# Kernel tuning notes

Measured on AMD Instinct MI355X. Metric: run time of the kernel, lower is better.

## Reference

```python
import jax, jax.numpy as jnp
import numpy as np

T, B, L, H, IN = 256, 64, 4, 1024, 1024


def setup_inputs() -> dict:
    key = jax.random.key(0)
    k1, k2, k3 = jax.random.split(key, 3)
    x = jax.random.normal(k1, (T, B, IN), dtype=jnp.float32)
    h = jnp.zeros((L, B, H), dtype=jnp.float32)
    # nn.Linear default init: U(-1/sqrt(fan_in), 1/sqrt(fan_in)), fan_in = IN + H
    bound = 1.0 / np.sqrt(IN + H)
    # Stacked per-layer weights: W[l] is [IN+H, 2H] (transposed vs torch), b[l] is [2H]
    W = jax.random.uniform(k2, (L, IN + H, 2 * H), dtype=jnp.float32, minval=-bound, maxval=bound)
    b = jax.random.uniform(k3, (L, 2 * H), dtype=jnp.float32, minval=-bound, maxval=bound)
    return {"x": x, "h": h, "W": W, "b": b}


def reference(x, h, W, b):
    """SRU-cell stacked RNN.
    x: [T, B, IN]; h: [L, B, H]; W: [L, IN+H, 2H]; b: [L, 2H].
    Returns (outputs [T, B, H], h_final [L*B, H]) matching the torch module
    (torch.cat(h, 0) concatenates layer states along the batch axis).
    """
    num_layers = W.shape[0]

    def step(hs, x_t):  # hs: [L, B, H], x_t: [B, IN]
        inp = x_t
        new_hs = []
        for i in range(num_layers):
            z = jnp.concatenate([inp, hs[i]], axis=-1) @ W[i] + b[i]  # [B, 2H]
            learn, forget = jnp.split(z, 2, axis=-1)
            f = jax.nn.sigmoid(forget)
            hn = f * hs[i] + (1.0 - f) * jnp.tanh(learn)  # [B, H]
            new_hs.append(hn)
            inp = hn  # cell output is both next-layer input and new hidden
        return jnp.stack(new_hs), inp

    h_final, outputs = jax.lax.scan(step, h, x)
    return outputs, h_final.reshape(-1, h_final.shape[-1])
```

## Files before the change

### kernel.cpp

```cpp
#include <hip/hip_runtime.h>


typedef _Float16 f16;
typedef _Float16 f16x8 __attribute__((ext_vector_type(8)));
typedef _Float16 f16x4 __attribute__((ext_vector_type(4)));
typedef float    floatx4 __attribute__((ext_vector_type(4)));

#define T_ 256
#define B_ 64
#define L_ 4
#define H_ 1024
#define IN_ 1024
#define K_ 2048

#define PANEL (B_*H_)
#define RING_BYTES ((size_t)L_*T_*PANEL*2)
#define CTRL_OFF   RING_BYTES
#define CTRL_BYTES 4096
#define X16_OFF    (CTRL_OFF + 65536)

__global__ void convert_x_kernel(const float* __restrict__ x, f16* __restrict__ x16) {
  const int nvec = (T_*B_*IN_)/4;
  const int stride = gridDim.x*blockDim.x;
  for (int v = blockIdx.x*blockDim.x + threadIdx.x; v < nvec; v += stride) {
    floatx4 in = ((const floatx4*)x)[v];
    f16x4 o; o.x = (f16)in.x; o.y = (f16)in.y; o.z = (f16)in.z; o.w = (f16)in.w;
    ((f16x4*)x16)[v] = o;
  }
}

template<int CSLP, int FSLP, bool SLACK>
__device__ __forceinline__ unsigned poll_bk(const unsigned int* line, unsigned tgt) {
  const unsigned int* p = line + (threadIdx.x & 63);
  unsigned v = __hip_atomic_load(p, __ATOMIC_RELAXED, __HIP_MEMORY_SCOPE_SYSTEM);
  if (!__all((int)(v >= tgt))) {
    __builtin_amdgcn_s_sleep(CSLP);
    for (;;) {
      v = __hip_atomic_load(p, __ATOMIC_RELAXED, __HIP_MEMORY_SCOPE_SYSTEM);
      if (__all((int)(v >= tgt))) break;
      __builtin_amdgcn_s_sleep(FSLP);
    }
  }
  unsigned a = tgt;
  if (SLACK) {
    if      (__all((int)(v >= tgt + 16))) a = tgt + 16;
    else if (__all((int)(v >= tgt + 4)))  a = tgt + 4;
    else if (__all((int)(v >= tgt + 1)))  a = tgt + 1;
  }
  asm volatile("" ::: "memory");
  return a;
}

__global__ __launch_bounds__(512, 2) void sru_main(
    const float* __restrict__ W,
    const float* __restrict__ bias,
    const f16*  __restrict__ x16,
    f16*        __restrict__ ring,
    unsigned int* __restrict__ done,
    float*      __restrict__ out)
{
  __shared__ f16 Wt[32][2048];
  __shared__ float red[2][4][2][64][4];
  __shared__ f16 hst[64][24];

  const int bid  = blockIdx.x;
  const int l    = bid >> 6;
  const int c    = bid & 63;
  const int n0   = c*16;
  const int tid  = threadIdx.x;
  const int lane = tid & 63;
  const int quad = lane >> 4;
  const int lc   = lane & 15;
  const int w    = tid >> 6;
  const int kh   = w & 1;
  const int mh   = (w >> 1) & 1;
  const int rh   = w >> 2;
  const int R    = rh*32 + mh*16;
  const int grp  = rh*2 + mh;

  {
    const int jj = tid & 15;
    const int k0 = tid >> 4;
    const int x0 = (jj & 7) << 3;
    const float* Wl = W + (size_t)l*K_*2048;
    for (int i = 0; i < 64; ++i) {
      int k = k0 + i*32;
      int ks = k ^ x0;
      Wt[jj][ks]      = (f16)Wl[(size_t)k*2048 + n0 + jj];
      Wt[16 + jj][ks] = (f16)Wl[(size_t)k*2048 + 1024 + n0 + jj];
    }
  }
  const float bl = bias[l*2048 + n0 + lc];
  const float bf = bias[l*2048 + 1024 + n0 + lc];
  __syncthreads();

  floatx4 hreg = 0.f;

  unsigned int* lineL = done + ((l*4 + grp) << 6);
  unsigned int* lineP = (l > 0) ? done + (((l-1)*4 + grp) << 6) : (unsigned int*)0;
  unsigned avail = 0;

  const int xr  = (lc & 7) << 3;
  const int sw0 = (quad*8) ^ xr;
  const int sw1 = (32 + quad*8) ^ xr;
  const int kb  = kh*1024;
  const f16* bL0 = &Wt[lc][sw0];
  const f16* bL1 = &Wt[lc][sw1];
  const f16* bF0 = &Wt[16 + lc][sw0];
  const f16* bF1 = &Wt[16 + lc][sw1];

  for (int t = 0; t < T_; ++t) {
    if (kh == 0) {
      if (l > 0 && avail < (unsigned)(t+1))
        avail = poll_bk<16, 4, true>(lineP, (unsigned)(t+1));
    } else {
      if (t > 0) (void)poll_bk<32, 4, false>(lineL, (unsigned)t);
    }

    floatx4 accLa = 0.f, accLb = 0.f, accFa = 0.f, accFb = 0.f;

    if (!(kh == 1 && t == 0)) {
      const f16* Abase;
      if (kh == 1)      Abase = ring + (size_t)(l*T_ + (t-1))*PANEL;
      else if (l == 0)  Abase = x16 + (size_t)t*PANEL;
      else              Abase = ring + (size_t)((l-1)*T_ + t)*PANEL;
      const f16* ap = Abase + (size_t)(R + lc)*H_ + quad*8;

      #pragma unroll
      for (int g = 0; g < 4; ++g) {
        floatx4 ar[8];
        #pragma unroll
        for (int j = 0; j < 8; ++j)
          ar[j] = *(const floatx4*)(ap + (g*8 + j)*32);
        #pragma unroll
        for (int j = 0; j < 8; ++j) {
          const int m = (g*8 + j) >> 1;
          const f16* pL = (j & 1) ? bL1 : bL0;
          const f16* pF = (j & 1) ? bF1 : bF0;
          f16x8 av = __builtin_bit_cast(f16x8, ar[j]);
          f16x8 bL = *(const f16x8*)(pL + kb + m*64);
          f16x8 bF = *(const f16x8*)(pF + kb + m*64);
          if (g & 1) {
            accLb = __builtin_amdgcn_mfma_f32_16x16x32_f16(av, bL, accLb, 0,0,0);
            accFb = __builtin_amdgcn_mfma_f32_16x16x32_f16(av, bF, accFb, 0,0,0);
          } else {
            accLa = __builtin_amdgcn_mfma_f32_16x16x32_f16(av, bL, accLa, 0,0,0);
            accFa = __builtin_amdgcn_mfma_f32_16x16x32_f16(av, bF, accFa, 0,0,0);
          }
        }
      }
    }

    if (kh == 1) {
      *(floatx4*)&red[t&1][grp][0][lane][0] = accLa + accLb;
      *(floatx4*)&red[t&1][grp][1][lane][0] = accFa + accFb;
    }
    __syncthreads();

    if (kh == 0) {
      floatx4 zL = accLa + accLb + *(const floatx4*)&red[t&1][grp][0][lane][0];
      floatx4 zF = accFa + accFb + *(const floatx4*)&red[t&1][grp][1][lane][0];
      f16* ringw = ring + (size_t)(l*T_ + t)*PANEL;

      #pragma unroll
      for (int r = 0; r < 4; ++r) {
        float zl = zL[r] + bl;
        float zf = zF[r] + bf;
        float fg = 1.0f/(1.0f + __expf(-zf));
        float th = 1.0f - 2.0f/(__expf(2.0f*zl) + 1.0f);
        float hn = fg*hreg[r] + (1.0f - fg)*th;
        hreg[r] = hn;
        hst[R + quad*4 + r][lc] = (f16)hn;
      }
      asm volatile("s_waitcnt lgkmcnt(0)" ::: "memory");
      __builtin_amdgcn_sched_barrier(0);

      if (lane < 32) {
        int srow = R + (lane >> 1);
        int sh   = lane & 1;
        floatx4 hv = *(const floatx4*)&hst[srow][sh*8];
        asm volatile("global_store_dwordx4 %0, %1, off sc0 sc1"
                     :: "v"((void*)(ringw + (size_t)srow*H_ + n0 + sh*8)),
                        "v"(hv) : "memory");
      }
      asm volatile("s_waitcnt vmcnt(0)" ::: "memory");
      if (lane == 0)
        __hip_atomic_store(lineL + c, (unsigned)(t+1),
                           __ATOMIC_RELAXED, __HIP_MEMORY_SCOPE_SYSTEM);

      if (l == 3) {
        #pragma unroll
        for (int r = 0; r < 4; ++r)
          out[(size_t)t*PANEL + (size_t)(R + quad*4 + r)*H_ + n0 + lc] = hreg[r];
      }
      if (t == T_ - 1) {
        #pragma unroll
        for (int r = 0; r < 4; ++r)
          out[(size_t)T_*PANEL + (size_t)l*PANEL + (size_t)(R + quad*4 + r)*H_ + n0 + lc] = hreg[r];
      }
    }
  }
}

extern "C" void kernel_launch(void* const* d_in, const int* in_sizes, int n_in,
                              void* d_out, int out_size, void* d_ws, size_t ws_size,
                              hipStream_t stream) {
  (void)in_sizes; (void)n_in; (void)out_size; (void)ws_size;
  const float* x = (const float*)d_in[0];
  const float* W = (const float*)d_in[2];
  const float* b = (const float*)d_in[3];
  float* out = (float*)d_out;

  char* ws = (char*)d_ws;
  f16* ring = (f16*)ws;
  unsigned int* done = (unsigned int*)(ws + CTRL_OFF);
  f16* x16 = (f16*)(ws + X16_OFF);

  hipMemsetAsync(ws + CTRL_OFF, 0, CTRL_BYTES, stream);
  convert_x_kernel<<<1024, 256, 0, stream>>>(x, x16);

  void* args[] = { (void*)&W, (void*)&b, (void*)&x16, (void*)&ring, (void*)&done, (void*)&out };
  hipLaunchCooperativeKernel((const void*)sru_main, dim3(256), dim3(512), args, 0, stream);
}
```

Measured before the change: 3.276 ms.

## Hold weight slices in registers and split K four ways per row pair

Each wave now keeps its 512-wide K slice of the learn and forget weights in VGPRs, loaded once from LDS. It processes two 16-row tiles with batched inline-asm global loads, instead of re-reading swizzled weights from LDS every step. Work is re-partitioned so four waves split K (two on the input, two on the recurrent state) per 32-row group, with a 3-way LDS reduction, and LDS is aliased between the weight staging area and the reduction buffers. This removes per-step LDS weight traffic and cuts the sync line count to two per layer. In exchange it raises register pressure, which may threaten 2 blocks/CU occupancy, and it serializes loads with an explicit vmcnt(0) wait.

```diff
diff --git a/kernel.cpp b/kernel.cpp
--- a/kernel.cpp
+++ b/kernel.cpp
@@ -51,6 +51,39 @@
   return a;
 }
 
+#define GLB_LOAD16(A, p)                                                     \
+  asm volatile(                                                              \
+    "global_load_dwordx4 %0, %16, off\n\t"                                   \
+    "global_load_dwordx4 %1, %16, off offset:64\n\t"                         \
+    "global_load_dwordx4 %2, %16, off offset:128\n\t"                        \
+    "global_load_dwordx4 %3, %16, off offset:192\n\t"                        \
+    "global_load_dwordx4 %4, %16, off offset:256\n\t"                        \
+    "global_load_dwordx4 %5, %16, off offset:320\n\t"                        \
+    "global_load_dwordx4 %6, %16, off offset:384\n\t"                        \
+    "global_load_dwordx4 %7, %16, off offset:448\n\t"                        \
+    "global_load_dwordx4 %8, %16, off offset:512\n\t"                        \
+    "global_load_dwordx4 %9, %16, off offset:576\n\t"                        \
+    "global_load_dwordx4 %10, %16, off offset:640\n\t"                       \
+    "global_load_dwordx4 %11, %16, off offset:704\n\t"                       \
+    "global_load_dwordx4 %12, %16, off offset:768\n\t"                       \
+    "global_load_dwordx4 %13, %16, off offset:832\n\t"                       \
+    "global_load_dwordx4 %14, %16, off offset:896\n\t"                       \
+    "global_load_dwordx4 %15, %16, off offset:960"                           \
+    : "=&v"(A[0]),"=&v"(A[1]),"=&v"(A[2]),"=&v"(A[3]),                       \
+      "=&v"(A[4]),"=&v"(A[5]),"=&v"(A[6]),"=&v"(A[7]),                       \
+      "=&v"(A[8]),"=&v"(A[9]),"=&v"(A[10]),"=&v"(A[11]),                     \
+      "=&v"(A[12]),"=&v"(A[13]),"=&v"(A[14]),"=&v"(A[15])                    \
+    : "v"((const void*)(p)) : "memory")
+
+#define WAITV0 do {                                                          \
+    asm volatile("s_waitcnt vmcnt(0)" ::: "memory");                         \
+    __builtin_amdgcn_sched_barrier(0);                                       \
+  } while (0)
+
+typedef f16   wt_t[32][2048];
+typedef float red_t[2][3][2][2][2][64][4];
+typedef f16   hst_t[64][24];
+
 __global__ __launch_bounds__(512, 2) void sru_main(
     const float* __restrict__ W,
     const float* __restrict__ bias,
@@ -59,9 +92,10 @@
     unsigned int* __restrict__ done,
     float*      __restrict__ out)
 {
-  __shared__ f16 Wt[32][2048];
-  __shared__ float red[2][4][2][64][4];
-  __shared__ f16 hst[64][24];
+  __shared__ __align__(16) char smem[131072];
+  wt_t&  Wt  = *reinterpret_cast<wt_t*>(smem);
+  red_t& red = *reinterpret_cast<red_t*>(smem);
+  hst_t& hst = *reinterpret_cast<hst_t*>(smem + sizeof(red_t));
 
   const int bid  = blockIdx.x;
   const int l    = bid >> 6;
@@ -72,110 +106,118 @@
   const int quad = lane >> 4;
   const int lc   = lane & 15;
   const int w    = tid >> 6;
-  const int kh   = w & 1;
-  const int mh   = (w >> 1) & 1;
+  const int kq   = w & 3;
   const int rh   = w >> 2;
-  const int R    = rh*32 + mh*16;
-  const int grp  = rh*2 + mh;
+  const int R    = rh*32;
 
   {
     const int jj = tid & 15;
     const int k0 = tid >> 4;
-    const int x0 = (jj & 7) << 3;
     const float* Wl = W + (size_t)l*K_*2048;
     for (int i = 0; i < 64; ++i) {
       int k = k0 + i*32;
-      int ks = k ^ x0;
-      Wt[jj][ks]      = (f16)Wl[(size_t)k*2048 + n0 + jj];
-      Wt[16 + jj][ks] = (f16)Wl[(size_t)k*2048 + 1024 + n0 + jj];
+      Wt[jj][k]      = (f16)Wl[(size_t)k*2048 + n0 + jj];
+      Wt[16 + jj][k] = (f16)Wl[(size_t)k*2048 + 1024 + n0 + jj];
     }
   }
   const float bl = bias[l*2048 + n0 + lc];
   const float bf = bias[l*2048 + 1024 + n0 + lc];
   __syncthreads();
 
-  floatx4 hreg = 0.f;
-
-  unsigned int* lineL = done + ((l*4 + grp) << 6);
-  unsigned int* lineP = (l > 0) ? done + (((l-1)*4 + grp) << 6) : (unsigned int*)0;
+  f16x8 bL[16], bF[16];
+  {
+    const int kw = kq*512 + quad*8;
+    #pragma unroll
+    for (int j = 0; j < 16; ++j) {
+      bL[j] = *(const f16x8*)&Wt[lc][kw + j*32];
+      bF[j] = *(const f16x8*)&Wt[16 + lc][kw + j*32];
+    }
+  }
+  __syncthreads();
+
+  floatx4 hreg0 = 0.f, hreg1 = 0.f;
+
+  const bool useH = (kq >= 2);
+  const int  aloc = (kq & 1)*512 + quad*8;
+
+  unsigned int* lineL = done + ((l*2 + rh) << 6);
+  unsigned int* lineP = (l > 0) ? done + (((l-1)*2 + rh) << 6) : (unsigned int*)0;
   unsigned avail = 0;
 
-  const int xr  = (lc & 7) << 3;
-  const int sw0 = (quad*8) ^ xr;
-  const int sw1 = (32 + quad*8) ^ xr;
-  const int kb  = kh*1024;
-  const f16* bL0 = &Wt[lc][sw0];
-  const f16* bL1 = &Wt[lc][sw1];
-  const f16* bF0 = &Wt[16 + lc][sw0];
-  const f16* bF1 = &Wt[16 + lc][sw1];
-
   for (int t = 0; t < T_; ++t) {
-    if (kh == 0) {
+    if (!useH) {
       if (l > 0 && avail < (unsigned)(t+1))
         avail = poll_bk<16, 4, true>(lineP, (unsigned)(t+1));
     } else {
       if (t > 0) (void)poll_bk<32, 4, false>(lineL, (unsigned)t);
     }
 
-    floatx4 accLa = 0.f, accLb = 0.f, accFa = 0.f, accFb = 0.f;
-
-    if (!(kh == 1 && t == 0)) {
+    floatx4 accL0 = 0.f, accL1 = 0.f, accF0 = 0.f, accF1 = 0.f;
+
+    if (!(useH && t == 0)) {
       const f16* Abase;
-      if (kh == 1)      Abase = ring + (size_t)(l*T_ + (t-1))*PANEL;
-      else if (l == 0)  Abase = x16 + (size_t)t*PANEL;
-      else              Abase = ring + (size_t)((l-1)*T_ + t)*PANEL;
-      const f16* ap = Abase + (size_t)(R + lc)*H_ + quad*8;
-
-      #pragma unroll
-      for (int g = 0; g < 4; ++g) {
-        floatx4 ar[8];
+      if (useH)        Abase = ring + (size_t)(l*T_ + (t-1))*PANEL;
+      else if (l == 0) Abase = x16 + (size_t)t*PANEL;
+      else             Abase = ring + (size_t)((l-1)*T_ + t)*PANEL;
+      const f16* ap0 = Abase + (size_t)(R + lc)*H_ + aloc;
+      const f16* ap1 = ap0 + 16*H_;
+
+      floatx4 ar[16];
+      GLB_LOAD16(ar, ap0);
+      WAITV0;
+      #pragma unroll
+      for (int j = 0; j < 16; ++j) {
+        f16x8 av = __builtin_bit_cast(f16x8, ar[j]);
+        accL0 = __builtin_amdgcn_mfma_f32_16x16x32_f16(av, bL[j], accL0, 0,0,0);
+        accF0 = __builtin_amdgcn_mfma_f32_16x16x32_f16(av, bF[j], accF0, 0,0,0);
+      }
+      GLB_LOAD16(ar, ap1);
+      WAITV0;
+      #pragma unroll
+      for (int j = 0; j < 16; ++j) {
+        f16x8 av = __builtin_bit_cast(f16x8, ar[j]);
+        accL1 = __builtin_amdgcn_mfma_f32_16x16x32_f16(av, bL[j], accL1, 0,0,0);
+        accF1 = __builtin_amdgcn_mfma_f32_16x16x32_f16(av, bF[j], accF1, 0,0,0);
+      }
+    }
+
+    if (kq != 0) {
+      const int s = kq - 1;
+      *(floatx4*)&red[t&1][s][rh][0][0][lane][0] = accL0;
+      *(floatx4*)&red[t&1][s][rh][0][1][lane][0] = accF0;
+      *(floatx4*)&red[t&1][s][rh][1][0][lane][0] = accL1;
+      *(floatx4*)&red[t&1][s][rh][1][1][lane][0] = accF1;
+    }
+    __syncthreads();
+
+    if (kq == 0) {
+      #pragma unroll
+      for (int s = 0; s < 3; ++s) {
+        accL0 += *(const floatx4*)&red[t&1][s][rh][0][0][lane][0];
+        accF0 += *(const floatx4*)&red[t&1][s][rh][0][1][lane][0];
+        accL1 += *(const floatx4*)&red[t&1][s][rh][1][0][lane][0];
+        accF1 += *(const floatx4*)&red[t&1][s][rh][1][1][lane][0];
+      }
+      f16* ringw = ring + (size_t)(l*T_ + t)*PANEL;
+
+      #pragma unroll
+      for (int rt = 0; rt < 2; ++rt) {
         #pragma unroll
-        for (int j = 0; j < 8; ++j)
-          ar[j] = *(const floatx4*)(ap + (g*8 + j)*32);
-        #pragma unroll
-        for (int j = 0; j < 8; ++j) {
-          const int m = (g*8 + j) >> 1;
-          const f16* pL = (j & 1) ? bL1 : bL0;
-          const f16* pF = (j & 1) ? bF1 : bF0;
-          f16x8 av = __builtin_bit_cast(f16x8, ar[j]);
-          f16x8 bL = *(const f16x8*)(pL + kb + m*64);
-          f16x8 bF = *(const f16x8*)(pF + kb + m*64);
-          if (g & 1) {
-            accLb = __builtin_amdgcn_mfma_f32_16x16x32_f16(av, bL, accLb, 0,0,0);
-            accFb = __builtin_amdgcn_mfma_f32_16x16x32_f16(av, bF, accFb, 0,0,0);
-          } else {
-            accLa = __builtin_amdgcn_mfma_f32_16x16x32_f16(av, bL, accLa, 0,0,0);
-            accFa = __builtin_amdgcn_mfma_f32_16x16x32_f16(av, bF, accFa, 0,0,0);
-          }
+        for (int r = 0; r < 4; ++r) {
+          float zl = (rt ? accL1[r] : accL0[r]) + bl;
+          float zf = (rt ? accF1[r] : accF0[r]) + bf;
+          float fg = 1.0f/(1.0f + __expf(-zf));
+          float th = 1.0f - 2.0f/(__expf(2.0f*zl) + 1.0f);
+          float hv = rt ? hreg1[r] : hreg0[r];
+          float hn = fg*hv + (1.0f - fg)*th;
+          if (rt) hreg1[r] = hn; else hreg0[r] = hn;
+          hst[R + rt*16 + quad*4 + r][lc] = (f16)hn;
         }
-      }
-    }
-
-    if (kh == 1) {
-      *(floatx4*)&red[t&1][grp][0][lane][0] = accLa + accLb;
-      *(floatx4*)&red[t&1][grp][1][lane][0] = accFa + accFb;
-    }
-    __syncthreads();
-
-    if (kh == 0) {
-      floatx4 zL = accLa + accLb + *(const floatx4*)&red[t&1][grp][0][lane][0];
-      floatx4 zF = accFa + accFb + *(const floatx4*)&red[t&1][grp][1][lane][0];
-      f16* ringw = ring + (size_t)(l*T_ + t)*PANEL;
-
-      #pragma unroll
-      for (int r = 0; r < 4; ++r) {
-        float zl = zL[r] + bl;
-        float zf = zF[r] + bf;
-        float fg = 1.0f/(1.0f + __expf(-zf));
-        float th = 1.0f - 2.0f/(__expf(2.0f*zl) + 1.0f);
-        float hn = fg*hreg[r] + (1.0f - fg)*th;
-        hreg[r] = hn;
-        hst[R + quad*4 + r][lc] = (f16)hn;
       }
       asm volatile("s_waitcnt lgkmcnt(0)" ::: "memory");
       __builtin_amdgcn_sched_barrier(0);
 
-      if (lane < 32) {
+      {
         int srow = R + (lane >> 1);
         int sh   = lane & 1;
         floatx4 hv = *(const floatx4*)&hst[srow][sh*8];
@@ -190,13 +232,20 @@
 
       if (l == 3) {
         #pragma unroll
-        for (int r = 0; r < 4; ++r)
-          out[(size_t)t*PANEL + (size_t)(R + quad*4 + r)*H_ + n0 + lc] = hreg[r];
+        for (int rt = 0; rt < 2; ++rt)
+          #pragma unroll
+          for (int r = 0; r < 4; ++r)
+            out[(size_t)t*PANEL + (size_t)(R + rt*16 + quad*4 + r)*H_ + n0 + lc]
+              = rt ? hreg1[r] : hreg0[r];
       }
       if (t == T_ - 1) {
         #pragma unroll
-        for (int r = 0; r < 4; ++r)
-          out[(size_t)T_*PANEL + (size_t)l*PANEL + (size_t)(R + quad*4 + r)*H_ + n0 + lc] = hreg[r];
+        for (int rt = 0; rt < 2; ++rt)
+          #pragma unroll
+          for (int r = 0; r < 4; ++r)
+            out[(size_t)T_*PANEL + (size_t)l*PANEL
+                + (size_t)(R + rt*16 + quad*4 + r)*H_ + n0 + lc]
+              = rt ? hreg1[r] : hreg0[r];
       }
     }
   }
```

Result: slower. 5.216 ms (+59.2%).
